# Kernel optimization log

Measured on AMD Instinct MI355X. Metric: run time of the kernel, lower is better.

Reference implementation:

```python
import jax, jax.numpy as jnp
import numpy as np

N = 131072      # total nodes (64 graphs x 2048 points)
E = 2097152     # edges (avg degree 16)
D_IN = 3
HID = 128
LAT = 64
POINTS = 2048


def setup_inputs() -> dict:
    key = jax.random.key(0)
    ks = jax.random.split(key, 11)
    def kaiming(k, fan_in, shape):
        return jax.random.normal(k, shape, dtype=jnp.float32) * np.sqrt(2.0 / fan_in)
    return {
        "x": jax.random.normal(ks[0], (N, D_IN), dtype=jnp.float32),
        "eps": jax.random.normal(ks[1], (N, LAT), dtype=jnp.float32),
        "W1": kaiming(ks[2], D_IN, (D_IN, HID)),
        "b1": jnp.zeros((HID,), jnp.float32),
        "W2": kaiming(ks[3], HID, (HID, 2 * LAT)),
        "b2": jnp.zeros((2 * LAT,), jnp.float32),
        "Wd1": kaiming(ks[4], LAT, (LAT, HID)),
        "bd1": jnp.zeros((HID,), jnp.float32),
        "Wd2": kaiming(ks[5], HID, (HID, D_IN)),
        "bd2": jnp.zeros((D_IN,), jnp.float32),
        "edge_index": jax.random.randint(ks[6], (2, E), 0, N, dtype=jnp.int64),
    }


def reference(x, eps, W1, b1, W2, b2, Wd1, bd1, Wd2, bd2, edge_index):
    row, col = edge_index[0], edge_index[1]  # messages flow row -> col
    # GCN symmetric normalization with self-loops: deg = in-degree + 1
    deg = jax.ops.segment_sum(jnp.ones((E,), x.dtype), col, num_segments=N) + 1.0
    dinv = jax.lax.rsqrt(deg)                 # [N]
    enorm = dinv[row] * dinv[col]             # [E] edge norm
    self_norm = (dinv * dinv)[:, None]        # [N,1] self-loop norm

    def gcn(h, W, b):
        hw = h @ W                                            # [N,F]
        agg = jax.ops.segment_sum(hw[row] * enorm[:, None], col, num_segments=N)
        return agg + hw * self_norm + b

    h = jax.nn.relu(gcn(x, W1, b1))
    h = gcn(h, W2, b2)
    mean, logvar = jnp.split(h, 2, axis=-1)   # [N,LAT] each
    z = mean + eps * jnp.exp(0.5 * logvar)    # reparameterize
    hd = jax.nn.relu(z @ Wd1 + bd1)
    recon = (hd @ Wd2 + bd2).reshape(-1, POINTS, D_IN)
    return recon, mean, logvar
```

## Files before the change

### kernel.cpp

```cpp
#include <hip/hip_runtime.h>
#include <hip/hip_bf16.h>

#define NN 131072
#define NE 2097152
#define DIN 3
#define HID 128
#define LAT 64
#define NBUCK 256
#define BSHIFT 9
#define CAP 10240

typedef __attribute__((ext_vector_type(8))) short short8;
typedef __attribute__((ext_vector_type(4))) float f32x4;
typedef __hip_bfloat16 bf16;

__device__ __forceinline__ float blo(unsigned v) {
    unsigned t = v << 16; float f; __builtin_memcpy(&f, &t, 4); return f;
}
__device__ __forceinline__ float bhi(unsigned v) {
    unsigned t = v & 0xffff0000u; float f; __builtin_memcpy(&f, &t, 4); return f;
}
__device__ __forceinline__ unsigned pack2(float a, float b) {
    __hip_bfloat162 t; t.x = __float2bfloat16(a); t.y = __float2bfloat16(b);
    unsigned u; __builtin_memcpy(&u, &t, 4); return u;
}
__device__ __forceinline__ short f2bs(float f) {
    bf16 b = __float2bfloat16(f);
    short s; __builtin_memcpy(&s, &b, 2); return s;
}

__global__ void k_detect(const int* __restrict__ ei, int* __restrict__ flag) {
    if (blockIdx.x == 0 && threadIdx.x == 0) {
        int z = 0;
        for (int i = 0; i < 16; ++i) z |= ei[2 * i + 1];
        *flag = (z == 0) ? 1 : 0;
    }
}

__device__ __forceinline__ int eidx(const int* __restrict__ ei, long long pos, int is64) {
    return is64 ? ei[2 * pos] : ei[pos];
}

__global__ __launch_bounds__(256) void k_bin(const int* __restrict__ ei,
                                             const int* __restrict__ flag,
                                             int* __restrict__ bcnt,
                                             unsigned* __restrict__ pairs) {
    __shared__ int cnt[NBUCK];
    __shared__ int base[NBUCK];
    __shared__ int gbase[NBUCK];
    __shared__ int sc[NBUCK];
    __shared__ unsigned lp[4096];
    __shared__ unsigned short lb[4096];
    int t = threadIdx.x;
    int is64 = *flag;
    long long e0 = (long long)blockIdx.x * 4096;
    for (int i = t; i < NBUCK; i += 256) cnt[i] = 0;
    __syncthreads();
    unsigned pr[16]; int pb[16]; int pp[16];
#pragma unroll
    for (int i = 0; i < 16; ++i) {
        long long e = e0 + i * 256 + t;
        int r = eidx(ei, e, is64);
        int c = eidx(ei, NE + e, is64);
        int b = c >> BSHIFT;
        pr[i] = ((unsigned)(c & 511) << 17) | (unsigned)r;
        pb[i] = b;
        pp[i] = atomicAdd(&cnt[b], 1);
    }
    __syncthreads();
    if (t < NBUCK) sc[t] = cnt[t];
    __syncthreads();
    for (int d = 1; d < NBUCK; d <<= 1) {
        int add = (t < NBUCK && t >= d) ? sc[t - d] : 0;
        __syncthreads();
        if (t < NBUCK) sc[t] += add;
        __syncthreads();
    }
    if (t < NBUCK) {
        base[t] = sc[t] - cnt[t];
        gbase[t] = atomicAdd(&bcnt[t], cnt[t]);
    }
    __syncthreads();
#pragma unroll
    for (int i = 0; i < 16; ++i) {
        int pos = base[pb[i]] + pp[i];
        lp[pos] = pr[i];
        lb[pos] = (unsigned short)pb[i];
    }
    __syncthreads();
    for (int j = t; j < 4096; j += 256) {
        int b = lb[j];
        int g = gbase[b] + (j - base[b]);
        if (g < CAP) pairs[(size_t)b * CAP + g] = lp[j];
    }
}

__global__ __launch_bounds__(256) void k_bdeg2(const int* __restrict__ bcnt,
                                               const unsigned* __restrict__ pairs,
                                               int* __restrict__ lofs,
                                               float* __restrict__ dinv,
                                               int* __restrict__ bsum) {
    __shared__ int dc[512];
    __shared__ int ps[256];
    int b = blockIdx.x, t = threadIdx.x;
    dc[t] = 0; dc[t + 256] = 0;
    __syncthreads();
    int n = min(bcnt[b], CAP);
    const unsigned* p = pairs + (size_t)b * CAP;
    for (int i = t; i < n; i += 256) atomicAdd(&dc[p[i] >> 17], 1);
    __syncthreads();
    int d0 = dc[2 * t], d1 = dc[2 * t + 1];
    ps[t] = d0 + d1;
    __syncthreads();
    for (int d = 1; d < 256; d <<= 1) {
        int v = (t >= d) ? ps[t - d] : 0;
        __syncthreads();
        ps[t] += v;
        __syncthreads();
    }
    int ebase = ps[t] - d0 - d1;
    lofs[b * 512 + 2 * t]     = ebase;
    lofs[b * 512 + 2 * t + 1] = ebase + d0;
    dinv[b * 512 + 2 * t]     = rsqrtf((float)d0 + 1.0f);
    dinv[b * 512 + 2 * t + 1] = rsqrtf((float)d1 + 1.0f);
    if (t == 255) bsum[b] = ps[255];
}

__global__ __launch_bounds__(256) void k_scan256(const int* __restrict__ bsum,
                                                 int* __restrict__ bbase,
                                                 int* __restrict__ off) {
    __shared__ int s[256];
    int t = threadIdx.x;
    int v0 = bsum[t];
    s[t] = v0;
    __syncthreads();
    for (int d = 1; d < 256; d <<= 1) {
        int v = (t >= d) ? s[t - d] : 0;
        __syncthreads();
        s[t] += v;
        __syncthreads();
    }
    bbase[t] = s[t] - v0;
    if (t == 255) off[NN] = s[255];
}

__global__ __launch_bounds__(256) void k_fillb2(const int* __restrict__ bcnt,
                                                const unsigned* __restrict__ pairs,
                                                const int* __restrict__ lofs,
                                                const int* __restrict__ bbase,
                                                int* __restrict__ off,
                                                int* __restrict__ csr_row) {
    __shared__ int cur[512];
    __shared__ int so[512];
    int b = blockIdx.x, t = threadIdx.x;
    int gb = bbase[b];
    for (int i = t; i < 512; i += 256) {
        int o = gb + lofs[b * 512 + i];
        so[i] = o;
        off[b * 512 + i] = o;
        cur[i] = 0;
    }
    __syncthreads();
    int n = min(bcnt[b], CAP);
    const unsigned* p = pairs + (size_t)b * CAP;
    for (int i = t; i < n; i += 256) {
        unsigned pr = p[i];
        int c9 = pr >> 17;
        int pos = atomicAdd(&cur[c9], 1);
        csr_row[so[c9] + pos] = (int)(pr & 0x1FFFFu);
    }
}

__global__ __launch_bounds__(256) void k_prep_xn(const float* __restrict__ x,
                                                 const float* __restrict__ dinv,
                                                 float4* __restrict__ xn) {
    int n = blockIdx.x * 256 + threadIdx.x;
    if (n >= NN) return;
    float d = dinv[n];
    float4 v;
    v.x = x[n * 3 + 0] * d;
    v.y = x[n * 3 + 1] * d;
    v.z = x[n * 3 + 2] * d;
    v.w = 0.f;
    xn[n] = v;
}

__global__ __launch_bounds__(256) void k_gather_x(const float4* __restrict__ xn,
                                                  const int* __restrict__ csr_row,
                                                  const int* __restrict__ off,
                                                  const float* __restrict__ dinv,
                                                  float4* __restrict__ xagg) {
    int n = blockIdx.x * 256 + threadIdx.x;
    if (n >= NN) return;
    int s0 = off[n], s1 = off[n + 1];
    float4 s = xn[n];
    float ax = s.x, ay = s.y, az = s.z;
    int k = s0;
    for (; k + 2 <= s1; k += 2) {
        float4 v0 = xn[csr_row[k]];
        float4 v1 = xn[csr_row[k + 1]];
        ax += v0.x + v1.x; ay += v0.y + v1.y; az += v0.z + v1.z;
    }
    if (k < s1) {
        float4 v0 = xn[csr_row[k]];
        ax += v0.x; ay += v0.y; az += v0.z;
    }
    float dn = dinv[n];
    float4 o; o.x = ax * dn; o.y = ay * dn; o.z = az * dn; o.w = 0.f;
    xagg[n] = o;
}

__global__ __launch_bounds__(256) void k_l1post(const float4* __restrict__ xagg,
                                                const float* __restrict__ W1,
                                                const float* __restrict__ b1,
                                                const float* __restrict__ dinv,
                                                bf16* __restrict__ hp) {
    __shared__ float w[DIN * HID];
    __shared__ float sb[HID];
    for (int i = threadIdx.x; i < DIN * HID; i += 256) w[i] = W1[i];
    if (threadIdx.x < HID) sb[threadIdx.x] = b1[threadIdx.x];
    __syncthreads();
    int idx = blockIdx.x * 256 + threadIdx.x;
    int n = idx >> 7, f = idx & 127;
    float4 xa = xagg[n];
    float v = xa.x * w[f] + xa.y * w[HID + f] + xa.z * w[2 * HID + f] + sb[f];
    v = fmaxf(v, 0.f) * dinv[n];
    hp[idx] = __float2bfloat16(v);
}

__global__ __launch_bounds__(256) void k_gather_h(const bf16* __restrict__ src,
                                                  const int* __restrict__ csr_row,
                                                  const int* __restrict__ off,
                                                  const float* __restrict__ dinv,
                                                  bf16* __restrict__ hpre) {
    int wave = (blockIdx.x * 256 + threadIdx.x) >> 6;
    int lane = threadIdx.x & 63;
    if (wave >= NN) return;
    int sub = lane >> 4, l16 = lane & 15;
    int s0 = off[wave], s1 = off[wave + 1];
    const uint4* s128 = (const uint4*)src;
    float ac[8] = {0.f, 0.f, 0.f, 0.f, 0.f, 0.f, 0.f, 0.f};
    int k = s0 + sub;
    for (; k + 4 < s1; k += 8) {
        int ra = csr_row[k], rb = csr_row[k + 4];
        uint4 va = s128[(size_t)ra * 16 + l16];
        uint4 vb = s128[(size_t)rb * 16 + l16];
        ac[0] += blo(va.x) + blo(vb.x);
        ac[1] += bhi(va.x) + bhi(vb.x);
        ac[2] += blo(va.y) + blo(vb.y);
        ac[3] += bhi(va.y) + bhi(vb.y);
        ac[4] += blo(va.z) + blo(vb.z);
        ac[5] += bhi(va.z) + bhi(vb.z);
        ac[6] += blo(va.w) + blo(vb.w);
        ac[7] += bhi(va.w) + bhi(vb.w);
    }
    if (k < s1) {
        int ra = csr_row[k];
        uint4 va = s128[(size_t)ra * 16 + l16];
        ac[0] += blo(va.x); ac[1] += bhi(va.x);
        ac[2] += blo(va.y); ac[3] += bhi(va.y);
        ac[4] += blo(va.z); ac[5] += bhi(va.z);
        ac[6] += blo(va.w); ac[7] += bhi(va.w);
    }
#pragma unroll
    for (int i = 0; i < 8; ++i) {
        ac[i] += __shfl_xor(ac[i], 16, 64);
        ac[i] += __shfl_xor(ac[i], 32, 64);
    }
    if (sub == 0) {
        uint4 hv = s128[(size_t)wave * 16 + l16];
        float dn = dinv[wave];
        float o0 = (ac[0] + blo(hv.x)) * dn;
        float o1 = (ac[1] + bhi(hv.x)) * dn;
        float o2 = (ac[2] + blo(hv.y)) * dn;
        float o3 = (ac[3] + bhi(hv.y)) * dn;
        float o4 = (ac[4] + blo(hv.z)) * dn;
        float o5 = (ac[5] + bhi(hv.z)) * dn;
        float o6 = (ac[6] + blo(hv.w)) * dn;
        float o7 = (ac[7] + bhi(hv.w)) * dn;
        uint4 ov;
        ov.x = pack2(o0, o1); ov.y = pack2(o2, o3);
        ov.z = pack2(o4, o5); ov.w = pack2(o6, o7);
        ((uint4*)hpre)[(size_t)wave * 16 + l16] = ov;
    }
}

__global__ __launch_bounds__(256) void k_prep_w2(const float* __restrict__ W2,
                                                 bf16* __restrict__ w2s) {
    int i = blockIdx.x * 256 + threadIdx.x;
    int k = i >> 7, n = i & 127;
    int dst = n * HID + ((((k >> 3) ^ (n & 7))) << 3) + (k & 7);
    w2s[dst] = __float2bfloat16(W2[i]);
}

__global__ __launch_bounds__(256) void k_prep_wd1(const float* __restrict__ Wd1,
                                                  bf16* __restrict__ w1t) {
    int i = blockIdx.x * 256 + threadIdx.x;
    int k = i >> 7, j = i & 127;
    int dst = j * 64 + (((k >> 3) ^ (j & 7)) << 3) + (k & 7);
    w1t[dst] = __float2bfloat16(Wd1[i]);
}

__global__ __launch_bounds__(256) void k_prep_wd2(const float* __restrict__ Wd2,
                                                  bf16* __restrict__ w2t) {
    int i = blockIdx.x * 256 + threadIdx.x;
    int d = i >> 7, k = i & 127;
    int dst = d * 128 + (((k >> 3) ^ (d & 7)) << 3) + (k & 7);
    w2t[dst] = __float2bfloat16(d < 3 ? Wd2[k * 3 + d] : 0.0f);
}

__global__ __launch_bounds__(256) void k_gemm2_split(const bf16* __restrict__ hpre,
                                                     const bf16* __restrict__ w2s,
                                                     const float* __restrict__ b2,
                                                     float* __restrict__ mean_o,
                                                     float* __restrict__ logvar_o) {
    __shared__ short lw[HID * HID];
    __shared__ float sb[HID];
    {
        const short8* s = (const short8*)w2s;
        short8* d = (short8*)lw;
        for (int i = threadIdx.x; i < HID * HID / 8; i += 256) d[i] = s[i];
        if (threadIdx.x < HID) sb[threadIdx.x] = b2[threadIdx.x];
    }
    __syncthreads();
    int lane = threadIdx.x & 63;
    int wid = threadIdx.x >> 6;
    int l15 = lane & 15;
    int kgrp = lane >> 4;
    int nodeA = blockIdx.x * 64 + wid * 16 + l15;
    const short* hrow = (const short*)(hpre + (size_t)nodeA * HID);
    short8 a[4];
#pragma unroll
    for (int ks = 0; ks < 4; ++ks)
        a[ks] = *(const short8*)(hrow + ks * 32 + kgrp * 8);
    f32x4 acc[8];
#pragma unroll
    for (int cb = 0; cb < 8; ++cb) acc[cb] = (f32x4){0.f, 0.f, 0.f, 0.f};
#pragma unroll
    for (int cb = 0; cb < 8; ++cb) {
        int bn = cb * 16 + l15;
        int swz = bn & 7;
        const short* brow = &lw[bn * HID];
#pragma unroll
        for (int ks = 0; ks < 4; ++ks) {
            int k8 = ks * 4 + kgrp;
            short8 bfr = *(const short8*)(brow + ((k8 ^ swz) << 3));
            acc[cb] = __builtin_amdgcn_mfma_f32_16x16x32_bf16(a[ks], bfr, acc[cb], 0, 0, 0);
        }
    }
    int mrow = blockIdx.x * 64 + wid * 16 + (kgrp << 2);
#pragma unroll
    for (int cb = 0; cb < 8; ++cb) {
        int col = cb * 16 + l15;
        float bb = sb[col];
#pragma unroll
        for (int r = 0; r < 4; ++r) {
            int node = mrow + r;
            float v = acc[cb][r] + bb;
            if (col < LAT) mean_o[(size_t)node * LAT + col] = v;
            else           logvar_o[(size_t)node * LAT + (col - LAT)] = v;
        }
    }
}

__global__ __launch_bounds__(256) void k_decoder(const float* __restrict__ mean,
                                                 const float* __restrict__ logvar,
                                                 const float* __restrict__ eps,
                                                 const bf16* __restrict__ w1t,
                                                 const float* __restrict__ bd1,
                                                 const bf16* __restrict__ w2t,
                                                 const float* __restrict__ bd2,
                                                 float* __restrict__ recon) {
    __shared__ short zb[64 * 64];
    __shared__ short w1l[128 * 64];
    __shared__ short w2l[16 * 128];
    __shared__ short hb[64 * 128];
    __shared__ float sb1[HID];
    int t = threadIdx.x;
    {
        const short8* s1p = (const short8*)w1t;
        short8* d1p = (short8*)w1l;
        for (int i = t; i < 128 * 64 / 8; i += 256) d1p[i] = s1p[i];
        const short8* s2p = (const short8*)w2t;
        short8* d2p = (short8*)w2l;
        for (int i = t; i < 16 * 128 / 8; i += 256) d2p[i] = s2p[i];
        if (t < HID) sb1[t] = bd1[t];
    }
    long long nb = (long long)blockIdx.x * 64;
    {
        int node = t >> 2, k0 = (t & 3) * 16;
        const float* mp = mean   + (nb + node) * LAT + k0;
        const float* lp = logvar + (nb + node) * LAT + k0;
        const float* ep = eps    + (nb + node) * LAT + k0;
        short zr[16];
#pragma unroll
        for (int i = 0; i < 16; i += 4) {
            float4 m  = *(const float4*)(mp + i);
            float4 lv = *(const float4*)(lp + i);
            float4 e4 = *(const float4*)(ep + i);
            zr[i + 0] = f2bs(m.x + e4.x * expf(0.5f * lv.x));
            zr[i + 1] = f2bs(m.y + e4.y * expf(0.5f * lv.y));
            zr[i + 2] = f2bs(m.z + e4.z * expf(0.5f * lv.z));
            zr[i + 3] = f2bs(m.w + e4.w * expf(0.5f * lv.w));
        }
        int swz = node & 7;
        short8* zrow = (short8*)(zb + node * 64);
        short8 c0, c1;
#pragma unroll
        for (int i = 0; i < 8; ++i) { c0[i] = zr[i]; c1[i] = zr[8 + i]; }
        int k8a = k0 >> 3;
        zrow[k8a ^ swz] = c0;
        zrow[(k8a + 1) ^ swz] = c1;
    }
    __syncthreads();
    int lane = t & 63, w = t >> 6;
    int l15 = lane & 15, kg = lane >> 4;
    int node = w * 16 + l15;
    int aswz = node & 7;
    const short8* zrow = (const short8*)(zb + node * 64);
    short8 a0 = zrow[kg ^ aswz];
    short8 a1 = zrow[(4 + kg) ^ aswz];
#pragma unroll
    for (int cb = 0; cb < 8; ++cb) {
        int j = cb * 16 + l15;
        const short8* brow = (const short8*)(w1l + j * 64);
        int bs = j & 7;
        f32x4 acc = (f32x4){0.f, 0.f, 0.f, 0.f};
        acc = __builtin_amdgcn_mfma_f32_16x16x32_bf16(a0, brow[kg ^ bs], acc, 0, 0, 0);
        acc = __builtin_amdgcn_mfma_f32_16x16x32_bf16(a1, brow[(4 + kg) ^ bs], acc, 0, 0, 0);
        float bj = sb1[j];
        int k8 = j >> 3;
#pragma unroll
        for (int r = 0; r < 4; ++r) {
            int nrow = w * 16 + kg * 4 + r;
            hb[nrow * 128 + (((k8) ^ (nrow & 7)) << 3) + (j & 7)] =
                f2bs(fmaxf(acc[r] + bj, 0.f));
        }
    }
    __syncthreads();
    f32x4 acc2 = (f32x4){0.f, 0.f, 0.f, 0.f};
    const short8* arow = (const short8*)(hb + node * 128);
    const short8* brow2 = (const short8*)(w2l + l15 * 128);
    int as = node & 7, bs2 = l15 & 7;
#pragma unroll
    for (int ks = 0; ks < 4; ++ks) {
        int k8 = ks * 4 + kg;
        acc2 = __builtin_amdgcn_mfma_f32_16x16x32_bf16(arow[k8 ^ as], brow2[k8 ^ bs2],
                                                       acc2, 0, 0, 0);
    }
    if (l15 < 3) {
        float bb = bd2[l15];
#pragma unroll
        for (int r = 0; r < 4; ++r) {
            long long nr = nb + w * 16 + kg * 4 + r;
            recon[nr * 3 + l15] = acc2[r] + bb;
        }
    }
}

extern "C" void kernel_launch(void* const* d_in, const int* in_sizes, int n_in,
                              void* d_out, int out_size, void* d_ws, size_t ws_size,
                              hipStream_t stream) {
    const float* x   = (const float*)d_in[0];
    const float* eps = (const float*)d_in[1];
    const float* W1  = (const float*)d_in[2];
    const float* b1  = (const float*)d_in[3];
    const float* W2  = (const float*)d_in[4];
    const float* b2  = (const float*)d_in[5];
    const float* Wd1 = (const float*)d_in[6];
    const float* bd1 = (const float*)d_in[7];
    const float* Wd2 = (const float*)d_in[8];
    const float* bd2 = (const float*)d_in[9];
    const int*   ei  = (const int*)d_in[10];

    float* out = (float*)d_out;
    const long long RECON = (long long)NN * DIN;
    float* mean_o   = out + RECON;
    float* logvar_o = out + RECON + (long long)NN * LAT;

    bf16*     A       = (bf16*)d_ws;
    bf16*     B       = A + (size_t)NN * HID;
    bf16*     w2s     = B + (size_t)NN * HID;
    int*      lofs    = (int*)(w2s + HID * HID);
    int*      off     = lofs + NN;
    float*    dinv    = (float*)(off + NN + 1);
    int*      csr_row = (int*)(dinv + NN);
    int*      bcnt    = csr_row + NE;
    unsigned* pairs   = (unsigned*)(bcnt + NBUCK);
    int*      bsum    = (int*)(pairs + (size_t)NBUCK * CAP);
    int*      bbase   = bsum + NBUCK;
    bf16*     w1t     = (bf16*)(bbase + NBUCK);
    bf16*     w2t     = w1t + 128 * 64;
    float4*   xn      = (float4*)(w2t + 16 * 128);
    float4*   xagg    = xn + NN;
    int*      flag    = (int*)(xagg + NN);

    k_detect<<<1, 64, 0, stream>>>(ei, flag);

    hipMemsetAsync(bcnt, 0, NBUCK * sizeof(int), stream);
    k_bin<<<NE / 4096, 256, 0, stream>>>(ei, flag, bcnt, pairs);
    k_bdeg2<<<NBUCK, 256, 0, stream>>>(bcnt, pairs, lofs, dinv, bsum);
    k_scan256<<<1, 256, 0, stream>>>(bsum, bbase, off);
    k_fillb2<<<NBUCK, 256, 0, stream>>>(bcnt, pairs, lofs, bbase, off, csr_row);

    k_prep_w2<<<HID * HID / 256, 256, 0, stream>>>(W2, w2s);
    k_prep_wd1<<<LAT * HID / 256, 256, 0, stream>>>(Wd1, w1t);
    k_prep_wd2<<<16 * HID / 256, 256, 0, stream>>>(Wd2, w2t);

    k_prep_xn<<<NN / 256, 256, 0, stream>>>(x, dinv, xn);
    k_gather_x<<<NN / 256, 256, 0, stream>>>(xn, csr_row, off, dinv, xagg);
    k_l1post<<<(NN * HID) / 256, 256, 0, stream>>>(xagg, W1, b1, dinv, B);

    k_gather_h<<<(NN * 64) / 256, 256, 0, stream>>>(B, csr_row, off, dinv, A);
    k_gemm2_split<<<NN / 64, 256, 0, stream>>>(A, w2s, b2, mean_o, logvar_o);

    k_decoder<<<NN / 64, 256, 0, stream>>>(mean_o, logvar_o, eps, w1t, bd1, w2t, bd2, out);
}
```

Baseline: 359.8 us.

## Fuse prep, layer-1 gather/transform, and gemm2+decoder kernels; unroll gather_h

Inlines the int64 detection into k_bin and merges the three weight-prep kernels with the xn prep into one launch. The layer-1 gather and per-feature transform now run in one kernel, with 16 lanes per node. The second GEMM is fused with the decoder, so mean/logvar no longer have to be read back from global memory. k_gather_h is unrolled to four outstanding row loads per lane and uses cheaper bf16 unpacking. Together these cut launch count and intermediate global traffic, at the cost of more shared memory per block in the fused decoder, which may lower occupancy.

Measured after the change: 308.9 us. 1.16x faster.

```diff
diff --git a/kernel.cpp b/kernel.cpp
--- a/kernel.cpp
+++ b/kernel.cpp
@@ -20,6 +20,9 @@
 __device__ __forceinline__ float bhi(unsigned v) {
     unsigned t = v & 0xffff0000u; float f; __builtin_memcpy(&f, &t, 4); return f;
 }
+__device__ __forceinline__ float uaf(unsigned v) {
+    float f; __builtin_memcpy(&f, &v, 4); return f;
+}
 __device__ __forceinline__ unsigned pack2(float a, float b) {
     __hip_bfloat162 t; t.x = __float2bfloat16(a); t.y = __float2bfloat16(b);
     unsigned u; __builtin_memcpy(&u, &t, 4); return u;
@@ -29,20 +32,11 @@
     short s; __builtin_memcpy(&s, &b, 2); return s;
 }
 
-__global__ void k_detect(const int* __restrict__ ei, int* __restrict__ flag) {
-    if (blockIdx.x == 0 && threadIdx.x == 0) {
-        int z = 0;
-        for (int i = 0; i < 16; ++i) z |= ei[2 * i + 1];
-        *flag = (z == 0) ? 1 : 0;
-    }
-}
-
 __device__ __forceinline__ int eidx(const int* __restrict__ ei, long long pos, int is64) {
     return is64 ? ei[2 * pos] : ei[pos];
 }
 
 __global__ __launch_bounds__(256) void k_bin(const int* __restrict__ ei,
-                                             const int* __restrict__ flag,
                                              int* __restrict__ bcnt,
                                              unsigned* __restrict__ pairs) {
     __shared__ int cnt[NBUCK];
@@ -52,7 +46,10 @@
     __shared__ unsigned lp[4096];
     __shared__ unsigned short lb[4096];
     int t = threadIdx.x;
-    int is64 = *flag;
+    int z = 0;
+#pragma unroll
+    for (int i = 0; i < 16; ++i) z |= ei[2 * i + 1];
+    int is64 = (z == 0);
     long long e0 = (long long)blockIdx.x * 4096;
     for (int i = t; i < NBUCK; i += 256) cnt[i] = 0;
     __syncthreads();
@@ -171,61 +168,88 @@
     }
 }
 
-__global__ __launch_bounds__(256) void k_prep_xn(const float* __restrict__ x,
-                                                 const float* __restrict__ dinv,
-                                                 float4* __restrict__ xn) {
-    int n = blockIdx.x * 256 + threadIdx.x;
-    if (n >= NN) return;
-    float d = dinv[n];
-    float4 v;
-    v.x = x[n * 3 + 0] * d;
-    v.y = x[n * 3 + 1] * d;
-    v.z = x[n * 3 + 2] * d;
-    v.w = 0.f;
-    xn[n] = v;
-}
-
-__global__ __launch_bounds__(256) void k_gather_x(const float4* __restrict__ xn,
-                                                  const int* __restrict__ csr_row,
-                                                  const int* __restrict__ off,
-                                                  const float* __restrict__ dinv,
-                                                  float4* __restrict__ xagg) {
-    int n = blockIdx.x * 256 + threadIdx.x;
-    if (n >= NN) return;
-    int s0 = off[n], s1 = off[n + 1];
-    float4 s = xn[n];
-    float ax = s.x, ay = s.y, az = s.z;
-    int k = s0;
-    for (; k + 2 <= s1; k += 2) {
-        float4 v0 = xn[csr_row[k]];
-        float4 v1 = xn[csr_row[k + 1]];
-        ax += v0.x + v1.x; ay += v0.y + v1.y; az += v0.z + v1.z;
-    }
-    if (k < s1) {
-        float4 v0 = xn[csr_row[k]];
-        ax += v0.x; ay += v0.y; az += v0.z;
-    }
-    float dn = dinv[n];
-    float4 o; o.x = ax * dn; o.y = ay * dn; o.z = az * dn; o.w = 0.f;
-    xagg[n] = o;
-}
-
-__global__ __launch_bounds__(256) void k_l1post(const float4* __restrict__ xagg,
-                                                const float* __restrict__ W1,
-                                                const float* __restrict__ b1,
-                                                const float* __restrict__ dinv,
-                                                bf16* __restrict__ hp) {
+#define W2S_END 16384
+#define WD1_END (W2S_END + 8192)
+#define WD2_END (WD1_END + 2048)
+__global__ __launch_bounds__(256) void k_prep(const float* __restrict__ W2,
+                                              const float* __restrict__ Wd1,
+                                              const float* __restrict__ Wd2,
+                                              const float* __restrict__ x,
+                                              const float* __restrict__ dinv,
+                                              bf16* __restrict__ w2s,
+                                              bf16* __restrict__ w1t,
+                                              bf16* __restrict__ w2t,
+                                              float4* __restrict__ xn) {
+    int i = blockIdx.x * 256 + threadIdx.x;
+    if (i < W2S_END) {
+        int k = i >> 7, n = i & 127;
+        int dst = n * HID + ((((k >> 3) ^ (n & 7))) << 3) + (k & 7);
+        w2s[dst] = __float2bfloat16(W2[i]);
+    } else if (i < WD1_END) {
+        int j2 = i - W2S_END;
+        int k = j2 >> 7, j = j2 & 127;
+        int dst = j * 64 + (((k >> 3) ^ (j & 7)) << 3) + (k & 7);
+        w1t[dst] = __float2bfloat16(Wd1[j2]);
+    } else if (i < WD2_END) {
+        int j2 = i - WD1_END;
+        int d = j2 >> 7, k = j2 & 127;
+        int dst = d * 128 + (((k >> 3) ^ (d & 7)) << 3) + (k & 7);
+        w2t[dst] = __float2bfloat16(d < 3 ? Wd2[k * 3 + d] : 0.0f);
+    } else {
+        int n = i - WD2_END;
+        float d = dinv[n];
+        float4 v;
+        v.x = x[n * 3 + 0] * d;
+        v.y = x[n * 3 + 1] * d;
+        v.z = x[n * 3 + 2] * d;
+        v.w = 0.f;
+        xn[n] = v;
+    }
+}
+
+__global__ __launch_bounds__(256) void k_l1(const float4* __restrict__ xn,
+                                            const int* __restrict__ csr_row,
+                                            const int* __restrict__ off,
+                                            const float* __restrict__ dinv,
+                                            const float* __restrict__ W1,
+                                            const float* __restrict__ b1,
+                                            bf16* __restrict__ hp) {
     __shared__ float w[DIN * HID];
     __shared__ float sb[HID];
-    for (int i = threadIdx.x; i < DIN * HID; i += 256) w[i] = W1[i];
-    if (threadIdx.x < HID) sb[threadIdx.x] = b1[threadIdx.x];
-    __syncthreads();
-    int idx = blockIdx.x * 256 + threadIdx.x;
-    int n = idx >> 7, f = idx & 127;
-    float4 xa = xagg[n];
-    float v = xa.x * w[f] + xa.y * w[HID + f] + xa.z * w[2 * HID + f] + sb[f];
-    v = fmaxf(v, 0.f) * dinv[n];
-    hp[idx] = __float2bfloat16(v);
+    int t = threadIdx.x;
+    for (int i = t; i < DIN * HID; i += 256) w[i] = W1[i];
+    if (t < HID) sb[t] = b1[t];
+    __syncthreads();
+    int node = blockIdx.x * 16 + (t >> 4);
+    int g = t & 15;
+    int s0 = off[node], s1 = off[node + 1];
+    float ax = 0.f, ay = 0.f, az = 0.f;
+    for (int k = s0 + g; k < s1; k += 16) {
+        float4 v = xn[csr_row[k]];
+        ax += v.x; ay += v.y; az += v.z;
+    }
+    if (g == 0) {
+        float4 s = xn[node];
+        ax += s.x; ay += s.y; az += s.z;
+    }
+#pragma unroll
+    for (int m = 1; m < 16; m <<= 1) {
+        ax += __shfl_xor(ax, m, 64);
+        ay += __shfl_xor(ay, m, 64);
+        az += __shfl_xor(az, m, 64);
+    }
+    float dn = dinv[node];
+    ax *= dn; ay *= dn; az *= dn;
+    unsigned o[4];
+#pragma unroll
+    for (int j = 0; j < 4; ++j) {
+        int f0 = g * 8 + j * 2;
+        float v0 = fmaxf(ax * w[f0]     + ay * w[HID + f0]     + az * w[2 * HID + f0]     + sb[f0],     0.f) * dn;
+        float v1 = fmaxf(ax * w[f0 + 1] + ay * w[HID + f0 + 1] + az * w[2 * HID + f0 + 1] + sb[f0 + 1], 0.f) * dn;
+        o[j] = pack2(v0, v1);
+    }
+    uint4 ov; ov.x = o[0]; ov.y = o[1]; ov.z = o[2]; ov.w = o[3];
+    ((uint4*)hp)[(size_t)node * 16 + g] = ov;
 }
 
 __global__ __launch_bounds__(256) void k_gather_h(const bf16* __restrict__ src,
@@ -238,46 +262,52 @@
     if (wave >= NN) return;
     int sub = lane >> 4, l16 = lane & 15;
     int s0 = off[wave], s1 = off[wave + 1];
+    float dn = dinv[wave];
     const uint4* s128 = (const uint4*)src;
-    float ac[8] = {0.f, 0.f, 0.f, 0.f, 0.f, 0.f, 0.f, 0.f};
+    float lo[4] = {0.f, 0.f, 0.f, 0.f};
+    float hi[4] = {0.f, 0.f, 0.f, 0.f};
     int k = s0 + sub;
-    for (; k + 4 < s1; k += 8) {
+    for (; k + 12 < s1; k += 16) {
         int ra = csr_row[k], rb = csr_row[k + 4];
+        int rc = csr_row[k + 8], rd = csr_row[k + 12];
         uint4 va = s128[(size_t)ra * 16 + l16];
         uint4 vb = s128[(size_t)rb * 16 + l16];
-        ac[0] += blo(va.x) + blo(vb.x);
-        ac[1] += bhi(va.x) + bhi(vb.x);
-        ac[2] += blo(va.y) + blo(vb.y);
-        ac[3] += bhi(va.y) + bhi(vb.y);
-        ac[4] += blo(va.z) + blo(vb.z);
-        ac[5] += bhi(va.z) + bhi(vb.z);
-        ac[6] += blo(va.w) + blo(vb.w);
-        ac[7] += bhi(va.w) + bhi(vb.w);
-    }
-    if (k < s1) {
+        uint4 vc = s128[(size_t)rc * 16 + l16];
+        uint4 vd = s128[(size_t)rd * 16 + l16];
+        lo[0] += uaf(va.x << 16) + uaf(vb.x << 16) + uaf(vc.x << 16) + uaf(vd.x << 16);
+        hi[0] += uaf(va.x) + uaf(vb.x) + uaf(vc.x) + uaf(vd.x);
+        lo[1] += uaf(va.y << 16) + uaf(vb.y << 16) + uaf(vc.y << 16) + uaf(vd.y << 16);
+        hi[1] += uaf(va.y) + uaf(vb.y) + uaf(vc.y) + uaf(vd.y);
+        lo[2] += uaf(va.z << 16) + uaf(vb.z << 16) + uaf(vc.z << 16) + uaf(vd.z << 16);
+        hi[2] += uaf(va.z) + uaf(vb.z) + uaf(vc.z) + uaf(vd.z);
+        lo[3] += uaf(va.w << 16) + uaf(vb.w << 16) + uaf(vc.w << 16) + uaf(vd.w << 16);
+        hi[3] += uaf(va.w) + uaf(vb.w) + uaf(vc.w) + uaf(vd.w);
+    }
+    for (; k < s1; k += 4) {
         int ra = csr_row[k];
         uint4 va = s128[(size_t)ra * 16 + l16];
-        ac[0] += blo(va.x); ac[1] += bhi(va.x);
-        ac[2] += blo(va.y); ac[3] += bhi(va.y);
-        ac[4] += blo(va.z); ac[5] += bhi(va.z);
-        ac[6] += blo(va.w); ac[7] += bhi(va.w);
-    }
-#pragma unroll
-    for (int i = 0; i < 8; ++i) {
-        ac[i] += __shfl_xor(ac[i], 16, 64);
-        ac[i] += __shfl_xor(ac[i], 32, 64);
+        lo[0] += uaf(va.x << 16); hi[0] += uaf(va.x);
+        lo[1] += uaf(va.y << 16); hi[1] += uaf(va.y);
+        lo[2] += uaf(va.z << 16); hi[2] += uaf(va.z);
+        lo[3] += uaf(va.w << 16); hi[3] += uaf(va.w);
+    }
+#pragma unroll
+    for (int i = 0; i < 4; ++i) {
+        lo[i] += __shfl_xor(lo[i], 16, 64);
+        lo[i] += __shfl_xor(lo[i], 32, 64);
+        hi[i] += __shfl_xor(hi[i], 16, 64);
+        hi[i] += __shfl_xor(hi[i], 32, 64);
     }
     if (sub == 0) {
         uint4 hv = s128[(size_t)wave * 16 + l16];
-        float dn = dinv[wave];
-        float o0 = (ac[0] + blo(hv.x)) * dn;
-        float o1 = (ac[1] + bhi(hv.x)) * dn;
-        float o2 = (ac[2] + blo(hv.y)) * dn;
-        float o3 = (ac[3] + bhi(hv.y)) * dn;
-        float o4 = (ac[4] + blo(hv.z)) * dn;
-        float o5 = (ac[5] + bhi(hv.z)) * dn;
-        float o6 = (ac[6] + blo(hv.w)) * dn;
-        float o7 = (ac[7] + bhi(hv.w)) * dn;
+        float o0 = (lo[0] + blo(hv.x)) * dn;
+        float o1 = (hi[0] + bhi(hv.x)) * dn;
+        float o2 = (lo[1] + blo(hv.y)) * dn;
+        float o3 = (hi[1] + bhi(hv.y)) * dn;
+        float o4 = (lo[2] + blo(hv.z)) * dn;
+        float o5 = (hi[2] + bhi(hv.z)) * dn;
+        float o6 = (lo[3] + blo(hv.w)) * dn;
+        float o7 = (hi[3] + bhi(hv.w)) * dn;
         uint4 ov;
         ov.x = pack2(o0, o1); ov.y = pack2(o2, o3);
         ov.z = pack2(o4, o5); ov.w = pack2(o6, o7);
@@ -285,166 +315,118 @@
     }
 }
 
-__global__ __launch_bounds__(256) void k_prep_w2(const float* __restrict__ W2,
-                                                 bf16* __restrict__ w2s) {
-    int i = blockIdx.x * 256 + threadIdx.x;
-    int k = i >> 7, n = i & 127;
-    int dst = n * HID + ((((k >> 3) ^ (n & 7))) << 3) + (k & 7);
-    w2s[dst] = __float2bfloat16(W2[i]);
-}
-
-__global__ __launch_bounds__(256) void k_prep_wd1(const float* __restrict__ Wd1,
-                                                  bf16* __restrict__ w1t) {
-    int i = blockIdx.x * 256 + threadIdx.x;
-    int k = i >> 7, j = i & 127;
-    int dst = j * 64 + (((k >> 3) ^ (j & 7)) << 3) + (k & 7);
-    w1t[dst] = __float2bfloat16(Wd1[i]);
-}
-
-__global__ __launch_bounds__(256) void k_prep_wd2(const float* __restrict__ Wd2,
-                                                  bf16* __restrict__ w2t) {
-    int i = blockIdx.x * 256 + threadIdx.x;
-    int d = i >> 7, k = i & 127;
-    int dst = d * 128 + (((k >> 3) ^ (d & 7)) << 3) + (k & 7);
-    w2t[dst] = __float2bfloat16(d < 3 ? Wd2[k * 3 + d] : 0.0f);
-}
-
-__global__ __launch_bounds__(256) void k_gemm2_split(const bf16* __restrict__ hpre,
-                                                     const bf16* __restrict__ w2s,
-                                                     const float* __restrict__ b2,
-                                                     float* __restrict__ mean_o,
-                                                     float* __restrict__ logvar_o) {
-    __shared__ short lw[HID * HID];
-    __shared__ float sb[HID];
+__global__ __launch_bounds__(256) void k_gemm2dec(const bf16* __restrict__ hpre,
+                                                  const bf16* __restrict__ w2s,
+                                                  const float* __restrict__ b2,
+                                                  const float* __restrict__ eps,
+                                                  const bf16* __restrict__ w1t,
+                                                  const float* __restrict__ bd1,
+                                                  const bf16* __restrict__ w2t,
+                                                  const float* __restrict__ bd2,
+                                                  float* __restrict__ mean_o,
+                                                  float* __restrict__ logvar_o,
+                                                  float* __restrict__ recon) {
+    __shared__ __align__(16) char smem[62464];
+    short* lw  = (short*)smem;
+    short* hb  = (short*)smem;
+    short* zb  = (short*)(smem + 32768);
+    short* w1l = (short*)(smem + 40960);
+    short* w2l = (short*)(smem + 57344);
+    float* sb  = (float*)(smem + 61440);
+    float* sb1 = (float*)(smem + 61952);
+    int t = threadIdx.x;
     {
         const short8* s = (const short8*)w2s;
         short8* d = (short8*)lw;
-        for (int i = threadIdx.x; i < HID * HID / 8; i += 256) d[i] = s[i];
-        if (threadIdx.x < HID) sb[threadIdx.x] = b2[threadIdx.x];
-    }
-    __syncthreads();
-    int lane = threadIdx.x & 63;
-    int wid = threadIdx.x >> 6;
-    int l15 = lane & 15;
-    int kgrp = lane >> 4;
-    int nodeA = blockIdx.x * 64 + wid * 16 + l15;
-    const short* hrow = (const short*)(hpre + (size_t)nodeA * HID);
-    short8 a[4];
-#pragma unroll
-    for (int ks = 0; ks < 4; ++ks)
-        a[ks] = *(const short8*)(hrow + ks * 32 + kgrp * 8);
-    f32x4 acc[8];
-#pragma unroll
-    for (int cb = 0; cb < 8; ++cb) acc[cb] = (f32x4){0.f, 0.f, 0.f, 0.f};
-#pragma unroll
-    for (int cb = 0; cb < 8; ++cb) {
-        int bn = cb * 16 + l15;
-        int swz = bn & 7;
-        const short* brow = &lw[bn * HID];
-#pragma unroll
-        for (int ks = 0; ks < 4; ++ks) {
-            int k8 = ks * 4 + kgrp;
-            short8 bfr = *(const short8*)(brow + ((k8 ^ swz) << 3));
-            acc[cb] = __builtin_amdgcn_mfma_f32_16x16x32_bf16(a[ks], bfr, acc[cb], 0, 0, 0);
-        }
-    }
-    int mrow = blockIdx.x * 64 + wid * 16 + (kgrp << 2);
-#pragma unroll
-    for (int cb = 0; cb < 8; ++cb) {
-        int col = cb * 16 + l15;
-        float bb = sb[col];
-#pragma unroll
-        for (int r = 0; r < 4; ++r) {
-            int node = mrow + r;
-            float v = acc[cb][r] + bb;
-            if (col < LAT) mean_o[(size_t)node * LAT + col] = v;
-            else           logvar_o[(size_t)node * LAT + (col - LAT)] = v;
-        }
-    }
-}
-
-__global__ __launch_bounds__(256) void k_decoder(const float* __restrict__ mean,
-                                                 const float* __restrict__ logvar,
-                                                 const float* __restrict__ eps,
-                                                 const bf16* __restrict__ w1t,
-                                                 const float* __restrict__ bd1,
-                                                 const bf16* __restrict__ w2t,
-                                                 const float* __restrict__ bd2,
-                                                 float* __restrict__ recon) {
-    __shared__ short zb[64 * 64];
-    __shared__ short w1l[128 * 64];
-    __shared__ short w2l[16 * 128];
-    __shared__ short hb[64 * 128];
-    __shared__ float sb1[HID];
-    int t = threadIdx.x;
-    {
+        for (int i = t; i < HID * HID / 8; i += 256) d[i] = s[i];
         const short8* s1p = (const short8*)w1t;
         short8* d1p = (short8*)w1l;
         for (int i = t; i < 128 * 64 / 8; i += 256) d1p[i] = s1p[i];
         const short8* s2p = (const short8*)w2t;
         short8* d2p = (short8*)w2l;
         for (int i = t; i < 16 * 128 / 8; i += 256) d2p[i] = s2p[i];
-        if (t < HID) sb1[t] = bd1[t];
-    }
+        if (t < HID) { sb[t] = b2[t]; sb1[t] = bd1[t]; }
+    }
+    __syncthreads();
+    int lane = t & 63;
+    int wid = t >> 6;
+    int l15 = lane & 15;
+    int kgrp = lane >> 4;
     long long nb = (long long)blockIdx.x * 64;
-    {
-        int node = t >> 2, k0 = (t & 3) * 16;
-        const float* mp = mean   + (nb + node) * LAT + k0;
-        const float* lp = logvar + (nb + node) * LAT + k0;
-        const float* ep = eps    + (nb + node) * LAT + k0;
-        short zr[16];
-#pragma unroll
-        for (int i = 0; i < 16; i += 4) {
-            float4 m  = *(const float4*)(mp + i);
-            float4 lv = *(const float4*)(lp + i);
-            float4 e4 = *(const float4*)(ep + i);
-            zr[i + 0] = f2bs(m.x + e4.x * expf(0.5f * lv.x));
-            zr[i + 1] = f2bs(m.y + e4.y * expf(0.5f * lv.y));
-            zr[i + 2] = f2bs(m.z + e4.z * expf(0.5f * lv.z));
-            zr[i + 3] = f2bs(m.w + e4.w * expf(0.5f * lv.w));
+
+    int nodeA = (int)nb + wid * 16 + l15;
+    const short* hrow = (const short*)(hpre + (size_t)nodeA * HID);
+    short8 a[4];
+#pragma unroll
+    for (int ks = 0; ks < 4; ++ks)
+        a[ks] = *(const short8*)(hrow + ks * 32 + kgrp * 8);
+    f32x4 acc[8];
+#pragma unroll
+    for (int cb = 0; cb < 8; ++cb) acc[cb] = (f32x4){0.f, 0.f, 0.f, 0.f};
+#pragma unroll
+    for (int cb = 0; cb < 8; ++cb) {
+        int bn = cb * 16 + l15;
+        int swz = bn & 7;
+        const short* brow = &lw[bn * HID];
+#pragma unroll
+        for (int ks = 0; ks < 4; ++ks) {
+            int k8 = ks * 4 + kgrp;
+            short8 bfr = *(const short8*)(brow + ((k8 ^ swz) << 3));
+            acc[cb] = __builtin_amdgcn_mfma_f32_16x16x32_bf16(a[ks], bfr, acc[cb], 0, 0, 0);
         }
-        int swz = node & 7;
-        short8* zrow = (short8*)(zb + node * 64);
-        short8 c0, c1;
-#pragma unroll
-        for (int i = 0; i < 8; ++i) { c0[i] = zr[i]; c1[i] = zr[8 + i]; }
-        int k8a = k0 >> 3;
-        zrow[k8a ^ swz] = c0;
-        zrow[(k8a + 1) ^ swz] = c1;
-    }
-    __syncthreads();
-    int lane = t & 63, w = t >> 6;
-    int l15 = lane & 15, kg = lane >> 4;
-    int node = w * 16 + l15;
+    }
+
+    int mrowL = wid * 16 + (kgrp << 2);
+#pragma unroll
+    for (int cb = 0; cb < 4; ++cb) {
+        int col = cb * 16 + l15;
+        float bm = sb[col], bl = sb[64 + col];
+#pragma unroll
+        for (int r = 0; r < 4; ++r) {
+            int nl = mrowL + r;
+            long long ng = nb + nl;
+            float m  = acc[cb][r] + bm;
+            float lv = acc[cb + 4][r] + bl;
+            mean_o[ng * LAT + col] = m;
+            logvar_o[ng * LAT + col] = lv;
+            float e = eps[ng * LAT + col];
+            float zv = m + e * expf(0.5f * lv);
+            zb[nl * 64 + (((col >> 3) ^ (nl & 7)) << 3) + (col & 7)] = f2bs(zv);
+        }
+    }
+    __syncthreads();
+
+    int node = wid * 16 + l15;
     int aswz = node & 7;
     const short8* zrow = (const short8*)(zb + node * 64);
-    short8 a0 = zrow[kg ^ aswz];
-    short8 a1 = zrow[(4 + kg) ^ aswz];
+    short8 a0 = zrow[kgrp ^ aswz];
+    short8 a1 = zrow[(4 + kgrp) ^ aswz];
 #pragma unroll
     for (int cb = 0; cb < 8; ++cb) {
         int j = cb * 16 + l15;
         const short8* brow = (const short8*)(w1l + j * 64);
         int bs = j & 7;
-        f32x4 acc = (f32x4){0.f, 0.f, 0.f, 0.f};
-        acc = __builtin_amdgcn_mfma_f32_16x16x32_bf16(a0, brow[kg ^ bs], acc, 0, 0, 0);
-        acc = __builtin_amdgcn_mfma_f32_16x16x32_bf16(a1, brow[(4 + kg) ^ bs], acc, 0, 0, 0);
+        f32x4 acc1 = (f32x4){0.f, 0.f, 0.f, 0.f};
+        acc1 = __builtin_amdgcn_mfma_f32_16x16x32_bf16(a0, brow[kgrp ^ bs], acc1, 0, 0, 0);
+        acc1 = __builtin_amdgcn_mfma_f32_16x16x32_bf16(a1, brow[(4 + kgrp) ^ bs], acc1, 0, 0, 0);
         float bj = sb1[j];
         int k8 = j >> 3;
 #pragma unroll
         for (int r = 0; r < 4; ++r) {
-            int nrow = w * 16 + kg * 4 + r;
-            hb[nrow * 128 + (((k8) ^ (nrow & 7)) << 3) + (j & 7)] =
-                f2bs(fmaxf(acc[r] + bj, 0.f));
+            int nrow = wid * 16 + kgrp * 4 + r;
+            hb[nrow * 128 + ((k8 ^ (nrow & 7)) << 3) + (j & 7)] =
+                f2bs(fmaxf(acc1[r] + bj, 0.f));
         }
     }
     __syncthreads();
+
     f32x4 acc2 = (f32x4){0.f, 0.f, 0.f, 0.f};
     const short8* arow = (const short8*)(hb + node * 128);
     const short8* brow2 = (const short8*)(w2l + l15 * 128);
     int as = node & 7, bs2 = l15 & 7;
 #pragma unroll
     for (int ks = 0; ks < 4; ++ks) {
-        int k8 = ks * 4 + kg;
+        int k8 = ks * 4 + kgrp;
         acc2 = __builtin_amdgcn_mfma_f32_16x16x32_bf16(arow[k8 ^ as], brow2[k8 ^ bs2],
                                                        acc2, 0, 0, 0);
     }
@@ -452,7 +434,7 @@
         float bb = bd2[l15];
 #pragma unroll
         for (int r = 0; r < 4; ++r) {
-            long long nr = nb + w * 16 + kg * 4 + r;
+            long long nr = nb + wid * 16 + kgrp * 4 + r;
             recon[nr * 3 + l15] = acc2[r] + bb;
         }
     }
@@ -492,27 +474,20 @@
     bf16*     w1t     = (bf16*)(bbase + NBUCK);
     bf16*     w2t     = w1t + 128 * 64;
     float4*   xn      = (float4*)(w2t + 16 * 128);
-    float4*   xagg    = xn + NN;
-    int*      flag    = (int*)(xagg + NN);
-
-    k_detect<<<1, 64, 0, stream>>>(ei, flag);
 
     hipMemsetAsync(bcnt, 0, NBUCK * sizeof(int), stream);
-    k_bin<<<NE / 4096, 256, 0, stream>>>(ei, flag, bcnt, pairs);
+    k_bin<<<NE / 4096, 256, 0, stream>>>(ei, bcnt, pairs);
     k_bdeg2<<<NBUCK, 256, 0, stream>>>(bcnt, pairs, lofs, dinv, bsum);
     k_scan256<<<1, 256, 0, stream>>>(bsum, bbase, off);
     k_fillb2<<<NBUCK, 256, 0, stream>>>(bcnt, pairs, lofs, bbase, off, csr_row);
 
-    k_prep_w2<<<HID * HID / 256, 256, 0, stream>>>(W2, w2s);
-    k_prep_wd1<<<LAT * HID / 256, 256, 0, stream>>>(Wd1, w1t);
-    k_prep_wd2<<<16 * HID / 256, 256, 0, stream>>>(Wd2, w2t);
-
-    k_prep_xn<<<NN / 256, 256, 0, stream>>>(x, dinv, xn);
-    k_gather_x<<<NN / 256, 256, 0, stream>>>(xn, csr_row, off, dinv, xagg);
-    k_l1post<<<(NN * HID) / 256, 256, 0, stream>>>(xagg, W1, b1, dinv, B);
+    k_prep<<<(WD2_END + NN) / 256, 256, 0, stream>>>(W2, Wd1, Wd2, x, dinv,
+                                                     w2s, w1t, w2t, xn);
+
+    k_l1<<<NN / 16, 256, 0, stream>>>(xn, csr_row, off, dinv, W1, b1, B);
 
     k_gather_h<<<(NN * 64) / 256, 256, 0, stream>>>(B, csr_row, off, dinv, A);
-    k_gemm2_split<<<NN / 64, 256, 0, stream>>>(A, w2s, b2, mean_o, logvar_o);
-
-    k_decoder<<<NN / 64, 256, 0, stream>>>(mean_o, logvar_o, eps, w1t, bd1, w2t, bd2, out);
-}
+
+    k_gemm2dec<<<NN / 64, 256, 0, stream>>>(A, w2s, b2, eps, w1t, bd1, w2t, bd2,
+                                            mean_o, logvar_o, out);
+}
```
